# Optimization experiments

Hardware: AMD Instinct MI355X
Metric: run time of the kernel (lower is better)

The kernel has to match this reference:

```python
import jax, jax.numpy as jnp
import numpy as np

N = 50000          # num nodes
E = 800000         # num edges
DIN = 128          # in_channels
C = 64             # out_channels per head
H = 2              # heads
ED = 32            # edge_dim


def setup_inputs() -> dict:
    key = jax.random.key(0)
    ks = jax.random.split(key, 12)
    s = 1.0 / np.sqrt(DIN)
    se = 1.0 / np.sqrt(ED)
    return {
        "x": jax.random.normal(ks[0], (N, DIN), dtype=jnp.float32),
        "edge_index": jax.random.randint(ks[1], (2, E), 0, N, dtype=jnp.int32),
        "edge_attr": jax.random.normal(ks[2], (E, ED), dtype=jnp.float32),
        "Wq": jax.random.uniform(ks[3], (DIN, H * C), jnp.float32, -s, s),
        "bq": jax.random.uniform(ks[4], (H * C,), jnp.float32, -s, s),
        "Wk": jax.random.uniform(ks[5], (DIN, H * C), jnp.float32, -s, s),
        "bk": jax.random.uniform(ks[6], (H * C,), jnp.float32, -s, s),
        "Wv": jax.random.uniform(ks[7], (DIN, H * C), jnp.float32, -s, s),
        "bv": jax.random.uniform(ks[8], (H * C,), jnp.float32, -s, s),
        "We": jax.random.uniform(ks[9], (ED, H * C), jnp.float32, -se, se),
        "Wskip": jax.random.uniform(ks[10], (DIN, H * C), jnp.float32, -s, s),
        "bskip": jax.random.uniform(ks[11], (H * C,), jnp.float32, -s, s),
    }


def reference(x, edge_index, edge_attr, Wq, bq, Wk, bk, Wv, bv, We, Wskip, bskip):
    src, dst = edge_index[0], edge_index[1]
    # node-level projections [N, H, C]
    q = (x @ Wq + bq).reshape(N, H, C)
    k = (x @ Wk + bk).reshape(N, H, C)
    v = (x @ Wv + bv).reshape(N, H, C)
    e = (edge_attr @ We).reshape(E, H, C)  # lin_edge, no bias

    # per-edge gather
    q_e = q[dst]              # [E, H, C]
    k_e = k[src] + e          # key gets edge features
    alpha = jnp.einsum("ehc,ehc->eh", q_e, k_e) / jnp.sqrt(jnp.float32(C))

    # segment softmax over incoming edges of each dst node
    m = jax.ops.segment_max(alpha, dst, num_segments=N)       # [N, H]
    alpha = jnp.exp(alpha - m[dst])
    denom = jax.ops.segment_sum(alpha, dst, num_segments=N)   # [N, H]
    alpha = alpha / (denom[dst] + 1e-16)

    # weighted aggregation of values (value also gets edge features)
    msg = (v[src] + e) * alpha[..., None]                     # [E, H, C]
    out = jax.ops.segment_sum(msg, dst, num_segments=N)       # [N, H, C]
    out = out.reshape(N, H * C)

    # root weight skip connection (concat=True, beta=False)
    return out + x @ Wskip + bskip
```

## Files before the change

kernel.cpp:

```cpp
#include <hip/hip_runtime.h>
#include <cstdint>

#define NN 50000
#define EE 800000
#define DINC 128
#define HC 128
#define EDC 32
#define CAP 64
#define GEMM_BLKS 3128
#define EDGE_BLKS 3125

typedef __attribute__((ext_vector_type(8))) short short8;
typedef __attribute__((ext_vector_type(4))) float floatx4;

__device__ __forceinline__ unsigned int pk2(float a, float b){
  unsigned int ua = __float_as_uint(a), ub = __float_as_uint(b);
  ua = (ua + 0x7FFFu + ((ua >> 16) & 1u)) >> 16;
  ub = (ub + 0x7FFFu + ((ub >> 16) & 1u)) & 0xFFFF0000u;
  return ua | ub;
}
__device__ __forceinline__ float bflo(unsigned int p){ return __uint_as_float(p << 16); }
__device__ __forceinline__ float bfhi(unsigned int p){ return __uint_as_float(p & 0xFFFF0000u); }

__device__ __forceinline__ short8 ld_afrag(const float* xr){
  float4 f0 = *(const float4*)xr;
  float4 f1 = *(const float4*)(xr + 4);
  uint4 u;
  u.x = pk2(f0.x, f0.y); u.y = pk2(f0.z, f0.w);
  u.z = pk2(f1.x, f1.y); u.w = pk2(f1.z, f1.w);
  return *(short8*)&u;
}

__global__ __launch_bounds__(256) void k_gemm(
    const float* __restrict__ x,
    const float* __restrict__ Wq, const float* __restrict__ bq,
    const float* __restrict__ Wk, const float* __restrict__ bk,
    const float* __restrict__ Wv, const float* __restrict__ bv,
    const float* __restrict__ Wsk, const float* __restrict__ bsk,
    unsigned int* __restrict__ qbf, unsigned int* __restrict__ kv,
    float* __restrict__ out)
{
  __shared__ unsigned int sw[128*68];
  float* facc = (float*)sw;

  const int tid = threadIdx.x;
  const int mat = blockIdx.x & 3;
  const int bm  = (blockIdx.x >> 2) * 64;
  const float* W  = (mat==0)?Wq:(mat==1)?Wk:(mat==2)?Wv:Wsk;
  const float* bi = (mat==0)?bq:(mat==1)?bk:(mat==2)?bv:bsk;

  for (int idx = tid; idx < 64*64; idx += 256){
    int kp = idx >> 6;
    int n2 = (idx & 63) * 2;
    float2 a = *(const float2*)(W + (2*kp)*HC + n2);
    float2 b = *(const float2*)(W + (2*kp+1)*HC + n2);
    sw[n2*68 + kp]     = pk2(a.x, b.x);
    sw[(n2+1)*68 + kp] = pk2(a.y, b.y);
  }
  __syncthreads();

  const int l = tid & 63, wid = tid >> 6;
  const int lm = l & 15, ks = l >> 4;
  const int n0 = wid * 32;

  const float* xrow[4];
  #pragma unroll
  for (int mt = 0; mt < 4; ++mt){
    int r = bm + mt*16 + lm; if (r > NN-1) r = NN-1;
    xrow[mt] = x + (size_t)r*DINC + ks*8;
  }

  floatx4 acc[4][2];
  #pragma unroll
  for (int mt=0;mt<4;mt++) for(int nt=0;nt<2;nt++) acc[mt][nt] = (floatx4){0.f,0.f,0.f,0.f};

  #pragma unroll
  for (int kb = 0; kb < 4; ++kb){
    short8 a[4], b[2];
    #pragma unroll
    for (int mt=0;mt<4;mt++) a[mt] = ld_afrag(xrow[mt] + kb*32);
    #pragma unroll
    for (int nt=0;nt<2;nt++)
      b[nt] = *(const short8*)(sw + (n0+nt*16+lm)*68 + kb*16 + ks*4);
    #pragma unroll
    for (int mt=0;mt<4;mt++)
      #pragma unroll
      for (int nt=0;nt<2;nt++)
        acc[mt][nt] = __builtin_amdgcn_mfma_f32_16x16x32_bf16(a[mt], b[nt], acc[mt][nt], 0, 0, 0);
  }
  __syncthreads();

  #pragma unroll
  for (int mt=0;mt<4;mt++)
    #pragma unroll
    for (int nt=0;nt<2;nt++)
      #pragma unroll
      for (int r=0;r<4;r++){
        int row = mt*16 + ks*4 + r;
        int col = n0 + nt*16 + lm;
        facc[row*132 + col] = acc[mt][nt][r];
      }
  __syncthreads();

  for (int idx = tid; idx < 64*64; idx += 256){
    int row = idx >> 6, cp = idx & 63;
    int gr = bm + row;
    if (gr >= NN) continue;
    float v0 = facc[row*132 + 2*cp]     + bi[2*cp];
    float v1 = facc[row*132 + 2*cp + 1] + bi[2*cp+1];
    if (mat == 0)      qbf[gr*64 + cp] = pk2(v0, v1);
    else if (mat == 1) kv[(size_t)gr*128 + 2*cp]     = pk2(v0, v1);
    else if (mat == 2) kv[(size_t)gr*128 + 2*cp + 1] = pk2(v0, v1);
    else *(float2*)(out + (size_t)gr*HC + 2*cp) = make_float2(v0, v1);
  }
}

__global__ __launch_bounds__(256) void k_prep(const int* __restrict__ ei,
    const float* __restrict__ eattr,
    int* __restrict__ cnt, int2* __restrict__ eidsrc,
    unsigned int* __restrict__ ebf)
{
  int e = blockIdx.x*256 + threadIdx.x;
  if (e >= EE) return;
  int d = ei[EE + e];
  int s = ei[e];
  int pos = atomicAdd(cnt + d, 1);
  if (pos < CAP) eidsrc[(size_t)d*CAP + pos] = make_int2(e, s);
  if (ebf){
    const float4* er = (const float4*)(eattr + (size_t)e*EDC);
    #pragma unroll
    for (int c = 0; c < 4; ++c){
      float4 f0 = er[2*c], f1 = er[2*c+1];
      uint4 o;
      o.x = pk2(f0.x, f0.y); o.y = pk2(f0.z, f0.w);
      o.z = pk2(f1.x, f1.y); o.w = pk2(f1.z, f1.w);
      *(uint4*)(ebf + (size_t)e*16 + 4*c) = o;
    }
  }
}

__global__ __launch_bounds__(256) void k_agg(
    const float* __restrict__ eattr, const unsigned int* __restrict__ ebf,
    const float* __restrict__ We,
    const unsigned int* __restrict__ qbf, const unsigned int* __restrict__ kv,
    const int* __restrict__ cnt, const int2* __restrict__ eidsrc,
    float* __restrict__ out)
{
  __shared__ unsigned int sWeTp[64*34];
  __shared__ unsigned int sWe2p[32*64];
  __shared__ float swea[8*64];

  const int tid = threadIdx.x;
  for (int idx = tid; idx < 2048; idx += 256){
    int jj = idx >> 7, col = idx & 127;
    sWeTp[(col & 63)*34 + (col >> 6)*17 + jj] =
        pk2(We[(2*jj)*HC + col], We[(2*jj+1)*HC + col]);
  }
  for (int idx = tid; idx < 2048; idx += 256){
    int j = idx >> 6, cp = idx & 63;
    sWe2p[j*64 + cp] = pk2(We[j*HC + 2*cp], We[j*HC + 2*cp + 1]);
  }
  __syncthreads();

  const int wid = tid >> 6, l = tid & 63;
  const int half = l >> 5, m = l & 31;
  const int h = m >> 4, mm = m & 15;
  const int node = blockIdx.x*8 + wid*2 + half;

  int deg = cnt[node]; if (deg > CAP) deg = CAP;
  const size_t beg = (size_t)node*CAP;
  const int dm1 = (deg > 0) ? deg - 1 : 0;
  int degO = __shfl_xor(deg, 32, 64);
  const int dmax = deg > degO ? deg : degO;

  uint2 qp = *(const uint2*)(qbf + node*64 + h*32 + 2*mm);
  float q0 = bflo(qp.x), q1 = bfhi(qp.x), q2 = bflo(qp.y), q3 = bfhi(qp.y);

  float P2x = 0.f, P2y = 0.f;
  {
    const unsigned int* qrow = qbf + node*64 + h*32;
    const unsigned int* wt = sWeTp + h*17 + mm;
    #pragma unroll 8
    for (int cc = 0; cc < 32; ++cc){
      unsigned int up = qrow[cc];
      unsigned int u0 = wt[(2*cc)*34];
      unsigned int u1 = wt[(2*cc+1)*34];
      P2x += bflo(up)*bflo(u0) + bfhi(up)*bflo(u1);
      P2y += bflo(up)*bfhi(u0) + bfhi(up)*bfhi(u1);
    }
  }

  float a0=0.f, a1=0.f, a2=0.f, a3=0.f;
  float wx=0.f, wy=0.f, den=0.f;

  for (int i = 0; i < dmax; i += 4){
    int2 es[4]; float2 ea[4]; uint4 kx[4];
    #pragma unroll
    for (int t = 0; t < 4; ++t){
      int it = i + t; it = it < dm1 ? it : dm1;
      es[t] = eidsrc[beg + it];
    }
    if (ebf){
      #pragma unroll
      for (int t = 0; t < 4; ++t){
        int eid = min(max(es[t].x, 0), EE-1);
        unsigned int u = ebf[(size_t)eid*16 + mm];
        ea[t] = make_float2(bflo(u), bfhi(u));
      }
    } else {
      #pragma unroll
      for (int t = 0; t < 4; ++t){
        int eid = min(max(es[t].x, 0), EE-1);
        ea[t] = *(const float2*)(eattr + (size_t)eid*EDC + 2*mm);
      }
    }
    #pragma unroll
    for (int t = 0; t < 4; ++t){
      int src = min(max(es[t].y, 0), NN-1);
      kx[t] = *(const uint4*)(kv + (size_t)src*128 + h*64 + 4*mm);
    }
    float p[4];
    #pragma unroll
    for (int t = 0; t < 4; ++t)
      p[t] = q0*bflo(kx[t].x) + q1*bfhi(kx[t].x)
           + q2*bflo(kx[t].z) + q3*bfhi(kx[t].z)
           + P2x*ea[t].x + P2y*ea[t].y;
    #pragma unroll
    for (int s = 1; s < 16; s <<= 1){
      #pragma unroll
      for (int t = 0; t < 4; ++t) p[t] += __shfl_xor(p[t], s, 64);
    }
    #pragma unroll
    for (int t = 0; t < 4; ++t){
      float al = ((i + t) < deg) ? __expf(p[t]*0.125f) : 0.f;
      den += al;
      a0 += al*bflo(kx[t].y); a1 += al*bfhi(kx[t].y);
      a2 += al*bflo(kx[t].w); a3 += al*bfhi(kx[t].w);
      wx += al*ea[t].x;       wy += al*ea[t].y;
    }
  }

  const int slot = wid*2 + half;
  *(float2*)(swea + slot*64 + h*32 + 2*mm) = make_float2(wx, wy);
  float e0=0.f, e1=0.f, e2=0.f, e3=0.f;
  {
    const float* sv = swea + slot*64 + h*32;
    const unsigned int* w2 = sWe2p + h*32 + 2*mm;
    #pragma unroll 8
    for (int j = 0; j < 32; ++j){
      float w = sv[j];
      uint2 u = *(const uint2*)(w2 + j*64);
      e0 += w*bflo(u.x); e1 += w*bfhi(u.x);
      e2 += w*bflo(u.y); e3 += w*bfhi(u.y);
    }
  }
  float rden = 1.0f/(den + 1e-16f);
  float4 sk = *(const float4*)(out + (size_t)node*HC + h*64 + 4*mm);
  float4 o;
  o.x = sk.x + (a0 + e0)*rden;
  o.y = sk.y + (a1 + e1)*rden;
  o.z = sk.z + (a2 + e2)*rden;
  o.w = sk.w + (a3 + e3)*rden;
  *(float4*)(out + (size_t)node*HC + h*64 + 4*mm) = o;
}

extern "C" void kernel_launch(void* const* d_in, const int* in_sizes, int n_in,
                              void* d_out, int out_size, void* d_ws, size_t ws_size,
                              hipStream_t stream)
{
  const float* x   = (const float*)d_in[0];
  const int*   ei  = (const int*)d_in[1];
  const float* ea  = (const float*)d_in[2];
  const float* Wq  = (const float*)d_in[3];
  const float* bq  = (const float*)d_in[4];
  const float* Wk  = (const float*)d_in[5];
  const float* bk  = (const float*)d_in[6];
  const float* Wv  = (const float*)d_in[7];
  const float* bv  = (const float*)d_in[8];
  const float* We  = (const float*)d_in[9];
  const float* Wsk = (const float*)d_in[10];
  const float* bsk = (const float*)d_in[11];
  float* out = (float*)d_out;

  char* ws = (char*)d_ws;
  unsigned int* qbf = (unsigned int*)(ws);
  unsigned int* kvu = (unsigned int*)(ws + 12800000);
  int* cnt = (int*)(ws + 38400000);
  int2* eidsrc = (int2*)(ws + 38600000);
  unsigned int* ebf = (ws_size >= 115600000ull)
                    ? (unsigned int*)(ws + 64200000)
                    : nullptr;

  hipMemsetAsync(cnt, 0, NN*sizeof(int), stream);
  k_gemm<<<GEMM_BLKS, 256, 0, stream>>>(x, Wq,bq, Wk,bk, Wv,bv, Wsk,bsk,
                                        qbf, kvu, out);
  k_prep<<<EDGE_BLKS, 256, 0, stream>>>(ei, ea, cnt, eidsrc, ebf);
  k_agg<<<6250, 256, 0, stream>>>(ea, ebf, We, qbf, kvu, cnt, eidsrc, out);
}
```

Measured before the change: 426.5 us.

## Build compact CSR with edge features scattered in dst order

Replaces the fixed-capacity per-node edge bucket with a compact CSR. Degrees are counted by extra blocks appended to the GEMM launch, offsets are assigned by atomic bump allocation, and a scatter kernel writes src ids and bf16 edge attributes in destination order. The aggregation kernel then reads edge features contiguously per node instead of gathering them by edge id, and it drops the CAP truncation. In exchange it adds two small kernels and an extra atomic pass, and the edge-feature scatter writes are random.

Measured after the change: 436.2 us. 2.3% more time.

```diff
diff --git a/kernel.cpp b/kernel.cpp
--- a/kernel.cpp
+++ b/kernel.cpp
@@ -37,11 +37,18 @@
     const float* __restrict__ Wk, const float* __restrict__ bk,
     const float* __restrict__ Wv, const float* __restrict__ bv,
     const float* __restrict__ Wsk, const float* __restrict__ bsk,
+    const int* __restrict__ ei, int* __restrict__ cnt,
     unsigned int* __restrict__ qbf, unsigned int* __restrict__ kv,
-    float* __restrict__ out)
+    float* __restrict__ out, const int do_count)
 {
   __shared__ unsigned int sw[128*68];
   float* facc = (float*)sw;
+
+  if (do_count && blockIdx.x >= GEMM_BLKS){
+    int e = (blockIdx.x - GEMM_BLKS)*256 + threadIdx.x;
+    if (e < EE) atomicAdd(cnt + ei[EE + e], 1);
+    return;
+  }
 
   const int tid = threadIdx.x;
   const int mat = blockIdx.x & 3;
@@ -115,10 +122,38 @@
   }
 }
 
-__global__ __launch_bounds__(256) void k_prep(const int* __restrict__ ei,
-    const float* __restrict__ eattr,
-    int* __restrict__ cnt, int2* __restrict__ eidsrc,
-    unsigned int* __restrict__ ebf)
+__global__ __launch_bounds__(256) void k_alloc(const int* __restrict__ cnt,
+    int* __restrict__ off, int* __restrict__ woff, int* __restrict__ top)
+{
+  int i = blockIdx.x*256 + threadIdx.x;
+  if (i < NN){
+    int o = atomicAdd(top, cnt[i]);
+    off[i] = o; woff[i] = o;
+  }
+}
+
+__global__ __launch_bounds__(256) void k_scat(const int* __restrict__ ei,
+    const float* __restrict__ eattr, int* __restrict__ woff,
+    int* __restrict__ src_csr, unsigned int* __restrict__ ea_csr)
+{
+  int e = blockIdx.x*256 + threadIdx.x;
+  if (e >= EE) return;
+  int d = ei[EE + e];
+  int pos = atomicAdd(woff + d, 1);
+  src_csr[pos] = ei[e];
+  const float4* er = (const float4*)(eattr + (size_t)e*EDC);
+  #pragma unroll
+  for (int c = 0; c < 4; ++c){
+    float4 f0 = er[2*c], f1 = er[2*c+1];
+    uint4 o;
+    o.x = pk2(f0.x, f0.y); o.y = pk2(f0.z, f0.w);
+    o.z = pk2(f1.x, f1.y); o.w = pk2(f1.z, f1.w);
+    *(uint4*)(ea_csr + (size_t)pos*16 + 4*c) = o;
+  }
+}
+
+__global__ __launch_bounds__(256) void k_prep_fb(const int* __restrict__ ei,
+    int* __restrict__ cnt, int2* __restrict__ eidsrc)
 {
   int e = blockIdx.x*256 + threadIdx.x;
   if (e >= EE) return;
@@ -126,25 +161,15 @@
   int s = ei[e];
   int pos = atomicAdd(cnt + d, 1);
   if (pos < CAP) eidsrc[(size_t)d*CAP + pos] = make_int2(e, s);
-  if (ebf){
-    const float4* er = (const float4*)(eattr + (size_t)e*EDC);
-    #pragma unroll
-    for (int c = 0; c < 4; ++c){
-      float4 f0 = er[2*c], f1 = er[2*c+1];
-      uint4 o;
-      o.x = pk2(f0.x, f0.y); o.y = pk2(f0.z, f0.w);
-      o.z = pk2(f1.x, f1.y); o.w = pk2(f1.z, f1.w);
-      *(uint4*)(ebf + (size_t)e*16 + 4*c) = o;
-    }
-  }
 }
 
 __global__ __launch_bounds__(256) void k_agg(
-    const float* __restrict__ eattr, const unsigned int* __restrict__ ebf,
+    const float* __restrict__ eattr, const unsigned int* __restrict__ ea_csr,
     const float* __restrict__ We,
     const unsigned int* __restrict__ qbf, const unsigned int* __restrict__ kv,
-    const int* __restrict__ cnt, const int2* __restrict__ eidsrc,
-    float* __restrict__ out)
+    const int* __restrict__ cnt, const int* __restrict__ off,
+    const int* __restrict__ src_csr, const int2* __restrict__ eidsrc,
+    const int mode, float* __restrict__ out)
 {
   __shared__ unsigned int sWeTp[64*34];
   __shared__ unsigned int sWe2p[32*64];
@@ -167,8 +192,9 @@
   const int h = m >> 4, mm = m & 15;
   const int node = blockIdx.x*8 + wid*2 + half;
 
-  int deg = cnt[node]; if (deg > CAP) deg = CAP;
-  const size_t beg = (size_t)node*CAP;
+  int deg = cnt[node];
+  if (!mode && deg > CAP) deg = CAP;
+  const int base = mode ? off[node] : node*CAP;
   const int dm1 = (deg > 0) ? deg - 1 : 0;
   int degO = __shfl_xor(deg, 32, 64);
   const int dmax = deg > degO ? deg : degO;
@@ -194,29 +220,36 @@
   float wx=0.f, wy=0.f, den=0.f;
 
   for (int i = 0; i < dmax; i += 4){
-    int2 es[4]; float2 ea[4]; uint4 kx[4];
-    #pragma unroll
-    for (int t = 0; t < 4; ++t){
-      int it = i + t; it = it < dm1 ? it : dm1;
-      es[t] = eidsrc[beg + it];
-    }
-    if (ebf){
+    int srcv[4]; float2 ea[4]; uint4 kx[4];
+    if (mode){
+      int it[4];
       #pragma unroll
       for (int t = 0; t < 4; ++t){
-        int eid = min(max(es[t].x, 0), EE-1);
-        unsigned int u = ebf[(size_t)eid*16 + mm];
+        int q = i + t; it[t] = q < dm1 ? q : dm1;
+        srcv[t] = src_csr[base + it[t]];
+      }
+      #pragma unroll
+      for (int t = 0; t < 4; ++t){
+        unsigned int u = ea_csr[(size_t)(base + it[t])*16 + mm];
         ea[t] = make_float2(bflo(u), bfhi(u));
       }
     } else {
+      int2 es[4];
+      #pragma unroll
+      for (int t = 0; t < 4; ++t){
+        int q = i + t; q = q < dm1 ? q : dm1;
+        es[t] = eidsrc[(size_t)base + q];
+      }
       #pragma unroll
       for (int t = 0; t < 4; ++t){
         int eid = min(max(es[t].x, 0), EE-1);
         ea[t] = *(const float2*)(eattr + (size_t)eid*EDC + 2*mm);
+        srcv[t] = es[t].y;
       }
     }
     #pragma unroll
     for (int t = 0; t < 4; ++t){
-      int src = min(max(es[t].y, 0), NN-1);
+      int src = min(max(srcv[t], 0), NN-1);
       kx[t] = *(const uint4*)(kv + (size_t)src*128 + h*64 + 4*mm);
     }
     float p[4];
@@ -285,15 +318,28 @@
   char* ws = (char*)d_ws;
   unsigned int* qbf = (unsigned int*)(ws);
   unsigned int* kvu = (unsigned int*)(ws + 12800000);
-  int* cnt = (int*)(ws + 38400000);
-  int2* eidsrc = (int2*)(ws + 38600000);
-  unsigned int* ebf = (ws_size >= 115600000ull)
-                    ? (unsigned int*)(ws + 64200000)
-                    : nullptr;
-
-  hipMemsetAsync(cnt, 0, NN*sizeof(int), stream);
-  k_gemm<<<GEMM_BLKS, 256, 0, stream>>>(x, Wq,bq, Wk,bk, Wv,bv, Wsk,bsk,
-                                        qbf, kvu, out);
-  k_prep<<<EDGE_BLKS, 256, 0, stream>>>(ei, ea, cnt, eidsrc, ebf);
-  k_agg<<<6250, 256, 0, stream>>>(ea, ebf, We, qbf, kvu, cnt, eidsrc, out);
-}
+  int* cnt  = (int*)(ws + 38400000);
+  int* off  = (int*)(ws + 38600000);
+  int* woff = (int*)(ws + 38800000);
+  int* top  = (int*)(ws + 39000000);
+
+  if (ws_size >= 93800000ull){
+    int* src_csr = (int*)(ws + 39200000);
+    unsigned int* ea_csr = (unsigned int*)(ws + 42400000);
+    hipMemsetAsync(cnt, 0, 600004, stream);
+    k_gemm<<<GEMM_BLKS + EDGE_BLKS, 256, 0, stream>>>(
+        x, Wq,bq, Wk,bk, Wv,bv, Wsk,bsk, ei, cnt, qbf, kvu, out, 1);
+    k_alloc<<<196, 256, 0, stream>>>(cnt, off, woff, top);
+    k_scat<<<EDGE_BLKS, 256, 0, stream>>>(ei, ea, woff, src_csr, ea_csr);
+    k_agg<<<6250, 256, 0, stream>>>(ea, ea_csr, We, qbf, kvu,
+                                    cnt, off, src_csr, nullptr, 1, out);
+  } else {
+    int2* eidsrc = (int2*)(ws + 39200000);
+    hipMemsetAsync(cnt, 0, NN*sizeof(int), stream);
+    k_gemm<<<GEMM_BLKS, 256, 0, stream>>>(
+        x, Wq,bq, Wk,bk, Wv,bv, Wsk,bsk, ei, cnt, qbf, kvu, out, 0);
+    k_prep_fb<<<EDGE_BLKS, 256, 0, stream>>>(ei, cnt, eidsrc);
+    k_agg<<<6250, 256, 0, stream>>>(ea, nullptr, We, qbf, kvu,
+                                    cnt, nullptr, nullptr, eidsrc, 0, out);
+  }
+}
```
